# Optimization experiments

Hardware: AMD Instinct MI355X
Metric: run time of the kernel (lower is better)

The kernel has to match this reference:

```python
import jax, jax.numpy as jnp
import numpy as np

H = 8          # num_heads
EPS = 1e-5     # nn.LayerNorm default eps


def _attn(x, kv, wq, bq, wk, bk, wv, bv, wo, bo):
    # x: [B, Nq, D] queries; kv: [B, Nk, D] keys/values. softmax over keys (dim=-1).
    B, Nq, D = x.shape
    Nk = kv.shape[1]
    d = D // H
    q = (x @ wq + bq).reshape(B, Nq, H, d).transpose(0, 2, 1, 3)   # [B,h,Nq,d]
    k = (kv @ wk + bk).reshape(B, Nk, H, d).transpose(0, 2, 1, 3)  # [B,h,Nk,d]
    v = (kv @ wv + bv).reshape(B, Nk, H, d).transpose(0, 2, 1, 3)  # [B,h,Nk,d]
    scores = jnp.einsum('bhqd,bhkd->bhqk', q, k) * (d ** -0.5)
    a = jax.nn.softmax(scores, axis=-1)                            # softmax_dim='keys'
    ctx = jnp.einsum('bhqk,bhkd->bhqd', a, v)
    ctx = ctx.transpose(0, 2, 1, 3).reshape(B, Nq, D)
    return ctx @ wo + bo


def _ln(x, g, b):
    mu = jnp.mean(x, axis=-1, keepdims=True)
    var = jnp.var(x, axis=-1, keepdims=True)  # biased, matches torch LayerNorm
    return (x - mu) * jax.lax.rsqrt(var + EPS) * g + b


def setup_inputs() -> dict:
    key = jax.random.key(0)
    B, Nq, Nk, D = 2, 2048, 4096, 512
    Hid = 4 * D
    ks = jax.random.split(key, 32)
    s = 0.02
    r = lambda i, shp: jax.random.normal(ks[i], shp, dtype=jnp.float32) * s
    inp = {
        'x': jax.random.normal(ks[0], (B, Nq, D), dtype=jnp.float32),
        'cross': jax.random.normal(ks[1], (B, Nk, D), dtype=jnp.float32),
        # cross-attention projections (stored as [in, out])
        'ca_wq': r(2, (D, D)), 'ca_bq': jnp.zeros((D,), jnp.float32),
        'ca_wk': r(3, (D, D)), 'ca_bk': jnp.zeros((D,), jnp.float32),
        'ca_wv': r(4, (D, D)), 'ca_bv': jnp.zeros((D,), jnp.float32),
        'ca_wo': r(5, (D, D)), 'ca_bo': jnp.zeros((D,), jnp.float32),
        # self-attention projections
        'sa_wq': r(6, (D, D)), 'sa_bq': jnp.zeros((D,), jnp.float32),
        'sa_wk': r(7, (D, D)), 'sa_bk': jnp.zeros((D,), jnp.float32),
        'sa_wv': r(8, (D, D)), 'sa_bv': jnp.zeros((D,), jnp.float32),
        'sa_wo': r(9, (D, D)), 'sa_bo': jnp.zeros((D,), jnp.float32),
        # layer norms
        'ln1_g': jnp.ones((D,), jnp.float32), 'ln1_b': jnp.zeros((D,), jnp.float32),
        'ln2_g': jnp.ones((D,), jnp.float32), 'ln2_b': jnp.zeros((D,), jnp.float32),
        # MLP
        'mlp_w1': r(10, (D, Hid)), 'mlp_b1': jnp.zeros((Hid,), jnp.float32),
        'mlp_w2': r(11, (Hid, D)), 'mlp_b2': jnp.zeros((D,), jnp.float32),
    }
    return inp


def reference(x, cross,
              ca_wq, ca_bq, ca_wk, ca_bk, ca_wv, ca_bv, ca_wo, ca_bo,
              sa_wq, sa_bq, sa_wk, sa_bk, sa_wv, sa_bv, sa_wo, sa_bo,
              ln1_g, ln1_b, ln2_g, ln2_b,
              mlp_w1, mlp_b1, mlp_w2, mlp_b2):
    # a) cross-attention
    xc = _attn(x, cross, ca_wq, ca_bq, ca_wk, ca_bk, ca_wv, ca_bv, ca_wo, ca_bo)
    # b,c) LN then self-attention (Q=K=V=ln1(xc))
    xn = _ln(xc, ln1_g, ln1_b)
    xs = _attn(xn, xn, sa_wq, sa_bq, sa_wk, sa_bk, sa_wv, sa_bv, sa_wo, sa_bo)
    # d) residual
    y = xc + xs
    # e,f) LN + GELU MLP (torch GELU default = exact erf)
    h1 = jax.nn.gelu(_ln(y, ln2_g, ln2_b) @ mlp_w1 + mlp_b1, approximate=False)
    z = h1 @ mlp_w2 + mlp_b2
    # g) residual
    return y + z
```

## Files before the change

kernel.cpp:

```cpp
#include <hip/hip_runtime.h>
#include <math.h>

typedef _Float16 f16;
typedef __attribute__((ext_vector_type(8))) _Float16 f16x8;
typedef __attribute__((ext_vector_type(4))) _Float16 f16x4;
typedef __attribute__((ext_vector_type(4))) float f32x4;
typedef __attribute__((ext_vector_type(2))) __fp16 h16x2;

#define QSCALE 0.1803368801111204f

__device__ __forceinline__ void gl_lds16(const f16* g, f16* l) {
    __builtin_amdgcn_global_load_lds((const __attribute__((address_space(1))) void*)g,
                                     (__attribute__((address_space(3))) void*)l, 16, 0, 0);
}

struct PrepArgs {
    const float* ws[10]; f16* wd[10];
    const float* x; f16* xh;
    const float* cross; f16* ch;
};
__global__ __launch_bounds__(256)
void prep_all(PrepArgs p) {
    __shared__ float t[32][33];
    int bid = blockIdx.x, tid = threadIdx.x;
    if (bid < 4096) {
        const float* W; f16* Wt; int K, N, nx, ky;
        if (bid < 2048) {
            int wi = bid >> 8, tl = bid & 255;
            W = p.ws[wi]; Wt = p.wd[wi]; K = 512; N = 512; nx = tl & 15; ky = tl >> 4;
        } else if (bid < 3072) {
            int tl = bid - 2048;
            W = p.ws[8]; Wt = p.wd[8]; K = 512; N = 2048; nx = tl & 63; ky = tl >> 6;
        } else {
            int tl = bid - 3072;
            W = p.ws[9]; Wt = p.wd[9]; K = 2048; N = 512; nx = tl & 15; ky = tl >> 4;
        }
        int tx = tid & 31, ty = tid >> 5;
        int n0 = nx * 32, k0 = ky * 32;
#pragma unroll
        for (int i = 0; i < 4; i++)
            t[ty + i * 8][tx] = W[(size_t)(k0 + ty + i * 8) * N + n0 + tx];
        __syncthreads();
#pragma unroll
        for (int i = 0; i < 4; i++)
            Wt[(size_t)(n0 + ty + i * 8) * K + k0 + tx] = (f16)t[tx][ty + i * 8];
    } else {
        const float* X; f16* Y; size_t cb;
        if (bid < 6144) { X = p.x; Y = p.xh; cb = bid - 4096; }
        else            { X = p.cross; Y = p.ch; cb = bid - 6144; }
        size_t i = (cb * 256 + tid) * 4;
        f32x4 v = *(const f32x4*)(X + i);
        f16x4 o;
        o[0] = (f16)v[0]; o[1] = (f16)v[1]; o[2] = (f16)v[2]; o[3] = (f16)v[3];
        *(f16x4*)(Y + i) = o;
    }
}

__global__ __launch_bounds__(256)
void transpose_v(const f16* __restrict__ Vh, f16* __restrict__ Vt, int Nk) {
    __shared__ f16 t[64][72];
    int bh = blockIdx.y, k0 = blockIdx.x * 64;
    int tid = threadIdx.x;
    int kr = tid >> 2, dc = (tid & 3) * 16;
    const f16* src = Vh + ((size_t)bh * Nk + k0 + kr) * 64 + dc;
    f16x8 a = *(const f16x8*)src;
    f16x8 b = *(const f16x8*)(src + 8);
    *(f16x8*)&t[kr][dc] = a;
    *(f16x8*)&t[kr][dc + 8] = b;
    __syncthreads();
    int dr = tid >> 2, kc = (tid & 3) * 16;
    f16x8 o0, o1;
#pragma unroll
    for (int j = 0; j < 8; j++) { o0[j] = t[kc + j][dr]; o1[j] = t[kc + 8 + j][dr]; }
    f16* dst = Vt + ((size_t)bh * 64 + dr) * Nk + k0 + kc;
    *(f16x8*)dst = o0;
    *(f16x8*)(dst + 8) = o1;
}

__global__ __launch_bounds__(128)
void layernorm_f16(const float* __restrict__ X, const float* __restrict__ g,
                   const float* __restrict__ bta, f16* __restrict__ Y)
{
    __shared__ float red[4];
    int row = blockIdx.x;
    int tid = threadIdx.x;
    const float* x = X + (size_t)row * 512;
    f32x4 v = *(const f32x4*)(x + tid * 4);
    float s  = v[0] + v[1] + v[2] + v[3];
    float ss = v[0] * v[0] + v[1] * v[1] + v[2] * v[2] + v[3] * v[3];
#pragma unroll
    for (int m = 1; m < 64; m <<= 1) {
        s  += __shfl_xor(s, m, 64);
        ss += __shfl_xor(ss, m, 64);
    }
    int wave = tid >> 6, lane = tid & 63;
    if (lane == 0) { red[wave * 2] = s; red[wave * 2 + 1] = ss; }
    __syncthreads();
    s = red[0] + red[2]; ss = red[1] + red[3];
    float mu  = s * (1.0f / 512);
    float var = ss * (1.0f / 512) - mu * mu;
    float inv = rsqrtf(var + 1e-5f);
    f32x4 gv = *(const f32x4*)(g + tid * 4);
    f32x4 bv = *(const f32x4*)(bta + tid * 4);
    f16x4 o;
#pragma unroll
    for (int i = 0; i < 4; i++) o[i] = (f16)((v[i] - mu) * inv * gv[i] + bv[i]);
    *(f16x4*)(Y + (size_t)row * 512 + tid * 4) = o;
}

__global__ __launch_bounds__(256)
void gemm_f16(const f16* __restrict__ A, const f16* __restrict__ Wt,
              const float* __restrict__ b0, const float* __restrict__ b1,
              const float* __restrict__ b2, const float* __restrict__ res,
              float* __restrict__ Cf32, f16* __restrict__ C16,
              f16* __restrict__ hm0, f16* __restrict__ hm1, f16* __restrict__ hm2,
              int N, int K, int NBshift, int fused, int act, float s0)
{
    __shared__ __align__(16) f16 As[2][128 * 64];
    __shared__ __align__(16) f16 Bs[2][128 * 64];
    int tid = threadIdx.x, lane = tid & 63, wave = tid >> 6;
    int quad = lane >> 4, ln16 = lane & 15;
    int wm = wave >> 1, wn = wave & 1;
    int bm0 = blockIdx.y * 128, bn0 = blockIdx.x * 128;

    f32x4 acc[4][4];
#pragma unroll
    for (int i = 0; i < 4; i++)
#pragma unroll
        for (int j = 0; j < 4; j++) acc[i][j] = (f32x4){0.f, 0.f, 0.f, 0.f};

    const f16* ag[4]; const f16* bg[4]; int Loff[4];
#pragma unroll
    for (int j = 0; j < 4; j++) {
        int L = tid + j * 256;
        int row = L >> 3, cc = (L & 7) ^ (row & 7);
        ag[j] = A  + (size_t)(bm0 + row) * K + cc * 8;
        bg[j] = Wt + (size_t)(bn0 + row) * K + cc * 8;
        Loff[j] = L * 8;
    }
    int sw0 = (quad ^ (ln16 & 7)) * 8, sw1 = ((4 + quad) ^ (ln16 & 7)) * 8;

#pragma unroll
    for (int j = 0; j < 4; j++) { gl_lds16(ag[j], &As[0][Loff[j]]); gl_lds16(bg[j], &Bs[0][Loff[j]]); }
#pragma unroll
    for (int j = 0; j < 4; j++) { ag[j] += 64; bg[j] += 64; }

    int cur = 0;
    for (int kt = 0; kt < K; kt += 64) {
        __syncthreads();
        if (kt + 64 < K) {
            int nxt = cur ^ 1;
#pragma unroll
            for (int j = 0; j < 4; j++) { gl_lds16(ag[j], &As[nxt][Loff[j]]); gl_lds16(bg[j], &Bs[nxt][Loff[j]]); }
#pragma unroll
            for (int j = 0; j < 4; j++) { ag[j] += 64; bg[j] += 64; }
        }
        const f16* Ac = As[cur]; const f16* Bc = Bs[cur];
#pragma unroll
        for (int h = 0; h < 2; h++) {
            int sw = h ? sw1 : sw0;
            f16x8 af[4], bf[4];
#pragma unroll
            for (int mt = 0; mt < 4; mt++)
                af[mt] = *(const f16x8*)&Ac[(wm * 64 + mt * 16 + ln16) * 64 + sw];
#pragma unroll
            for (int nt = 0; nt < 4; nt++)
                bf[nt] = *(const f16x8*)&Bc[(wn * 64 + nt * 16 + ln16) * 64 + sw];
#pragma unroll
            for (int mt = 0; mt < 4; mt++)
#pragma unroll
                for (int nt = 0; nt < 4; nt++)
                    acc[mt][nt] = __builtin_amdgcn_mfma_f32_16x16x32_f16(af[mt], bf[nt], acc[mt][nt], 0, 0, 0);
        }
        cur ^= 1;
    }

    int NB = 1 << NBshift;
#pragma unroll
    for (int mt = 0; mt < 4; mt++) {
#pragma unroll
        for (int nt = 0; nt < 4; nt++) {
            int row = bm0 + wm * 64 + mt * 16 + quad * 4;
            int col = bn0 + wn * 64 + nt * 16 + ln16;
            float bv;
            if (fused) {
                int seg = col >> 9;
                const float* bp = seg == 0 ? b0 : (seg == 1 ? b1 : b2);
                bv = bp[col & 511];
            } else bv = b0[col];
#pragma unroll
            for (int i = 0; i < 4; i++) {
                int r = row + i;
                float v = acc[mt][nt][i] + bv;
                size_t idx = (size_t)r * N + col;
                if (res) v += res[idx];
                if (act) v = 0.5f * v * (1.0f + erff(v * 0.70710678118654752f));
                if (Cf32) Cf32[idx] = v;
                if (C16) C16[idx] = (f16)v;
                if (hm0) {
                    int seg = col >> 9;
                    f16* hp = seg == 0 ? hm0 : (seg == 1 ? hm1 : hm2);
                    float vv = seg == 0 ? v * s0 : v;
                    int hh = (col >> 6) & 7, d = col & 63;
                    int bt = r >> NBshift, rr = r & (NB - 1);
                    hp[(((size_t)bt * 8 + hh) * NB + rr) * 64 + d] = (f16)vv;
                }
            }
        }
    }
}

__global__ __launch_bounds__(256)
void gemm64(const f16* __restrict__ A, const f16* __restrict__ Wt,
            const float* __restrict__ bias, const float* __restrict__ res,
            float* __restrict__ Cf32, f16* __restrict__ hm0,
            int N, int K, int NBshift, float s0)
{
    __shared__ __align__(16) f16 As[2][64 * 64];
    __shared__ __align__(16) f16 Bs[2][64 * 64];
    int tid = threadIdx.x, lane = tid & 63, wave = tid >> 6;
    int quad = lane >> 4, ln16 = lane & 15;
    int wm = wave >> 1, wn = wave & 1;
    int bm0 = blockIdx.y * 64, bn0 = blockIdx.x * 64;

    f32x4 acc[2][2];
#pragma unroll
    for (int i = 0; i < 2; i++)
#pragma unroll
        for (int j = 0; j < 2; j++) acc[i][j] = (f32x4){0.f, 0.f, 0.f, 0.f};

    const f16* ag[2]; const f16* bg[2]; int Loff[2];
#pragma unroll
    for (int j = 0; j < 2; j++) {
        int L = tid + j * 256;
        int row = L >> 3, cc = (L & 7) ^ (row & 7);
        ag[j] = A  + (size_t)(bm0 + row) * K + cc * 8;
        bg[j] = Wt + (size_t)(bn0 + row) * K + cc * 8;
        Loff[j] = L * 8;
    }
    int sw0 = (quad ^ (ln16 & 7)) * 8, sw1 = ((4 + quad) ^ (ln16 & 7)) * 8;

#pragma unroll
    for (int j = 0; j < 2; j++) { gl_lds16(ag[j], &As[0][Loff[j]]); gl_lds16(bg[j], &Bs[0][Loff[j]]); }
#pragma unroll
    for (int j = 0; j < 2; j++) { ag[j] += 64; bg[j] += 64; }

    int cur = 0;
    for (int kt = 0; kt < K; kt += 64) {
        __syncthreads();
        if (kt + 64 < K) {
            int nxt = cur ^ 1;
#pragma unroll
            for (int j = 0; j < 2; j++) { gl_lds16(ag[j], &As[nxt][Loff[j]]); gl_lds16(bg[j], &Bs[nxt][Loff[j]]); }
#pragma unroll
            for (int j = 0; j < 2; j++) { ag[j] += 64; bg[j] += 64; }
        }
        const f16* Ac = As[cur]; const f16* Bc = Bs[cur];
#pragma unroll
        for (int h = 0; h < 2; h++) {
            int sw = h ? sw1 : sw0;
            f16x8 af[2], bf[2];
#pragma unroll
            for (int mt = 0; mt < 2; mt++)
                af[mt] = *(const f16x8*)&Ac[(wm * 32 + mt * 16 + ln16) * 64 + sw];
#pragma unroll
            for (int nt = 0; nt < 2; nt++)
                bf[nt] = *(const f16x8*)&Bc[(wn * 32 + nt * 16 + ln16) * 64 + sw];
#pragma unroll
            for (int mt = 0; mt < 2; mt++)
#pragma unroll
                for (int nt = 0; nt < 2; nt++)
                    acc[mt][nt] = __builtin_amdgcn_mfma_f32_16x16x32_f16(af[mt], bf[nt], acc[mt][nt], 0, 0, 0);
        }
        cur ^= 1;
    }

    int NB = 1 << NBshift;
#pragma unroll
    for (int mt = 0; mt < 2; mt++) {
#pragma unroll
        for (int nt = 0; nt < 2; nt++) {
            int row = bm0 + wm * 32 + mt * 16 + quad * 4;
            int col = bn0 + wn * 32 + nt * 16 + ln16;
            float bv = bias[col];
#pragma unroll
            for (int i = 0; i < 4; i++) {
                int r = row + i;
                float v = acc[mt][nt][i] + bv;
                size_t idx = (size_t)r * N + col;
                if (res) v += res[idx];
                if (Cf32) Cf32[idx] = v;
                if (hm0) {
                    int hh = (col >> 6) & 7, d = col & 63;
                    int bt = r >> NBshift, rr = r & (NB - 1);
                    hm0[(((size_t)bt * 8 + hh) * NB + rr) * 64 + d] = (f16)(v * s0);
                }
            }
        }
    }
}

__global__ __launch_bounds__(512, 4)
void attention_split(const f16* __restrict__ Qh, const f16* __restrict__ Kh,
                     const f16* __restrict__ Vt, f16* __restrict__ Op,
                     float* __restrict__ Lsum, int Nk)
{
    __shared__ __align__(16) f16 Kt[2][64 * 64];
    __shared__ __align__(16) f16 Vs[2][64 * 64];
    int z = blockIdx.z, b = z >> 2, sp = z & 3;
    int h = blockIdx.y, bh = b * 8 + h;
    int Nkh = Nk >> 2;
    int tid = threadIdx.x, lane = tid & 63, wave = tid >> 6;
    int quad = lane >> 4, ln16 = lane & 15, l7 = ln16 & 7;
    int qrow0 = blockIdx.x * 256 + wave * 32;

    f16x8 qf[2][2];
#pragma unroll
    for (int qh = 0; qh < 2; qh++)
#pragma unroll
        for (int dh = 0; dh < 2; dh++)
            qf[qh][dh] = *(const f16x8*)(Qh + ((size_t)bh * 2048 + qrow0 + qh * 16 + ln16) * 64
                                         + dh * 32 + quad * 8);
    f16x4 ones4;
#pragma unroll
    for (int j = 0; j < 4; j++) ones4[j] = (f16)1.0f;

    f32x4 oacc[2][4], aol[2];
#pragma unroll
    for (int qh = 0; qh < 2; qh++) {
        aol[qh] = (f32x4){0.f, 0.f, 0.f, 0.f};
#pragma unroll
        for (int dt = 0; dt < 4; dt++) oacc[qh][dt] = (f32x4){0.f, 0.f, 0.f, 0.f};
    }

    const f16* kb = Kh + ((size_t)bh * Nk + sp * Nkh) * 64;
    const f16* vb = Vt + (size_t)bh * 64 * Nk + sp * Nkh;

    const f16* kg; const f16* vg; int Lo;
    {
        int L = tid;
        int row = L >> 3, cc = (L & 7) ^ (row & 7);
        kg = kb + (size_t)row * 64 + cc * 8;
        vg = vb + (size_t)row * Nk + cc * 8;
        Lo = L * 8;
    }

    int koff[4][2], voff16[4][4];
#pragma unroll
    for (int nt = 0; nt < 4; nt++)
#pragma unroll
        for (int dh = 0; dh < 2; dh++)
            koff[nt][dh] = (nt * 16 + ln16) * 64 + ((dh * 4 + quad) ^ l7) * 8;
#pragma unroll
    for (int dt = 0; dt < 4; dt++)
#pragma unroll
        for (int nt = 0; nt < 4; nt++)
            voff16[dt][nt] = (dt * 16 + ln16) * 64 + (((nt * 2 + (quad >> 1)) ^ l7) * 8) + (quad & 1) * 4;

    gl_lds16(kg, &Kt[0][Lo]);
    gl_lds16(vg, &Vs[0][Lo]);
    kg += 64 * 64; vg += 64;

    int cur = 0;
    for (int kt = 0; kt < Nkh; kt += 64) {
        __syncthreads();
        if (kt + 64 < Nkh) {
            int nxt = cur ^ 1;
            gl_lds16(kg, &Kt[nxt][Lo]);
            gl_lds16(vg, &Vs[nxt][Lo]);
            kg += 64 * 64; vg += 64;
        }
        const f16* Ktc = Kt[cur]; const f16* Vsc = Vs[cur];

        f16x4 pk[2][4];
        {
            f16x8 kf[4][2];
#pragma unroll
            for (int nt = 0; nt < 4; nt++)
#pragma unroll
                for (int dh = 0; dh < 2; dh++)
                    kf[nt][dh] = *(const f16x8*)&Ktc[koff[nt][dh]];
#pragma unroll
            for (int qh = 0; qh < 2; qh++)
#pragma unroll
                for (int nt = 0; nt < 4; nt++) {
                    f32x4 zz = (f32x4){0.f, 0.f, 0.f, 0.f};
                    zz = __builtin_amdgcn_mfma_f32_16x16x32_f16(kf[nt][0], qf[qh][0], zz, 0, 0, 0);
                    zz = __builtin_amdgcn_mfma_f32_16x16x32_f16(kf[nt][1], qf[qh][1], zz, 0, 0, 0);
                    h16x2 pa = __builtin_amdgcn_cvt_pkrtz(exp2f(zz[0]), exp2f(zz[1]));
                    h16x2 pb = __builtin_amdgcn_cvt_pkrtz(exp2f(zz[2]), exp2f(zz[3]));
                    union { h16x2 h[2]; f16x4 v; } u;
                    u.h[0] = pa; u.h[1] = pb;
                    pk[qh][nt] = u.v;
                }
        }
        {
            f16x4 vf[4][4];
#pragma unroll
            for (int dt = 0; dt < 4; dt++)
#pragma unroll
                for (int nt = 0; nt < 4; nt++)
                    vf[dt][nt] = *(const f16x4*)&Vsc[voff16[dt][nt]];
#pragma unroll
            for (int qh = 0; qh < 2; qh++) {
#pragma unroll
                for (int nt = 0; nt < 4; nt++)
                    aol[qh] = __builtin_amdgcn_mfma_f32_16x16x16f16(ones4, pk[qh][nt], aol[qh], 0, 0, 0);
#pragma unroll
                for (int dt = 0; dt < 4; dt++)
#pragma unroll
                    for (int nt = 0; nt < 4; nt++)
                        oacc[qh][dt] = __builtin_amdgcn_mfma_f32_16x16x16f16(vf[dt][nt], pk[qh][nt], oacc[qh][dt], 0, 0, 0);
            }
        }
        cur ^= 1;
    }

#pragma unroll
    for (int qh = 0; qh < 2; qh++) {
        size_t rowb = ((size_t)(sp * 16 + bh) * 2048 + qrow0 + qh * 16 + ln16) * 64;
#pragma unroll
        for (int dt = 0; dt < 4; dt++) {
            f16x4 o4;
#pragma unroll
            for (int i = 0; i < 4; i++) o4[i] = (f16)oacc[qh][dt][i];
            *(f16x4*)&Op[rowb + dt * 16 + quad * 4] = o4;
        }
        if (quad == 0)
            Lsum[(size_t)(sp * 16 + bh) * 2048 + qrow0 + qh * 16 + ln16] = aol[qh][0];
    }
}

__global__ __launch_bounds__(256)
void attn_combine(const f16* __restrict__ Op, const float* __restrict__ Lsum,
                  f16* __restrict__ O)
{
    int t = blockIdx.x * 256 + threadIdx.x;
    int d = t & 63;
    int q = (t >> 6) & 2047;
    int bh = t >> 17;
    int b = bh >> 3, h = bh & 7;
    float l = 0.f, val = 0.f;
#pragma unroll
    for (int s = 0; s < 4; s++) {
        l   += Lsum[(size_t)(s * 16 + bh) * 2048 + q];
        val += (float)Op[((size_t)(s * 16 + bh) * 2048 + q) * 64 + d];
    }
    O[((size_t)b * 2048 + q) * 512 + h * 64 + d] = (f16)(val / l);
}

extern "C" void kernel_launch(void* const* d_in, const int* in_sizes, int n_in,
                              void* d_out, int out_size, void* d_ws, size_t ws_size,
                              hipStream_t stream)
{
    (void)in_sizes; (void)n_in; (void)out_size; (void)ws_size;
    const float* x      = (const float*)d_in[0];
    const float* cross  = (const float*)d_in[1];
    const float* ca_wq  = (const float*)d_in[2];
    const float* ca_bq  = (const float*)d_in[3];
    const float* ca_wk  = (const float*)d_in[4];
    const float* ca_bk  = (const float*)d_in[5];
    const float* ca_wv  = (const float*)d_in[6];
    const float* ca_bv  = (const float*)d_in[7];
    const float* ca_wo  = (const float*)d_in[8];
    const float* ca_bo  = (const float*)d_in[9];
    const float* sa_wq  = (const float*)d_in[10];
    const float* sa_bq  = (const float*)d_in[11];
    const float* sa_wk  = (const float*)d_in[12];
    const float* sa_bk  = (const float*)d_in[13];
    const float* sa_wv  = (const float*)d_in[14];
    const float* sa_bv  = (const float*)d_in[15];
    const float* sa_wo  = (const float*)d_in[16];
    const float* sa_bo  = (const float*)d_in[17];
    const float* ln1_g  = (const float*)d_in[18];
    const float* ln1_b  = (const float*)d_in[19];
    const float* ln2_g  = (const float*)d_in[20];
    const float* ln2_b  = (const float*)d_in[21];
    const float* mlp_w1 = (const float*)d_in[22];
    const float* mlp_b1 = (const float*)d_in[23];
    const float* mlp_w2 = (const float*)d_in[24];
    const float* mlp_b2 = (const float*)d_in[25];
    float* out = (float*)d_out;

    float* XC = (float*)d_ws;
    float* Yb = XC + 2097152;
    f16* fb   = (f16*)(Yb + 2097152);
    f16* xh     = fb;
    f16* crossh = xh + 2097152;
    f16* xnh    = crossh + 4194304;
    f16* xn2h   = xnh + 2097152;
    f16* Qh     = xn2h + 2097152;
    f16* Kh     = Qh + 2097152;
    f16* Vh     = Kh + 4194304;
    f16* Vtb    = Vh + 4194304;
    f16* ctxh   = Vtb + 4194304;
    f16* h1h    = ctxh + 2097152;
    f16* t_caq  = h1h + 8388608;
    f16* t_cak  = t_caq + 262144;
    f16* t_cav  = t_cak + 262144;
    f16* t_cao  = t_cav + 262144;
    f16* t_saq  = t_cao + 262144;
    f16* t_sak  = t_saq + 262144;
    f16* t_sav  = t_sak + 262144;
    f16* t_sao  = t_sav + 262144;
    f16* t_w1   = t_sao + 262144;
    f16* t_w2   = t_w1 + 1048576;
    float* Lsum = (float*)(t_w2 + 1048576);

    PrepArgs pa;
    pa.ws[0] = ca_wq; pa.wd[0] = t_caq;
    pa.ws[1] = ca_wk; pa.wd[1] = t_cak;
    pa.ws[2] = ca_wv; pa.wd[2] = t_cav;
    pa.ws[3] = ca_wo; pa.wd[3] = t_cao;
    pa.ws[4] = sa_wq; pa.wd[4] = t_saq;
    pa.ws[5] = sa_wk; pa.wd[5] = t_sak;
    pa.ws[6] = sa_wv; pa.wd[6] = t_sav;
    pa.ws[7] = sa_wo; pa.wd[7] = t_sao;
    pa.ws[8] = mlp_w1; pa.wd[8] = t_w1;
    pa.ws[9] = mlp_w2; pa.wd[9] = t_w2;
    pa.x = x; pa.xh = xh; pa.cross = cross; pa.ch = crossh;
    prep_all<<<10240, 256, 0, stream>>>(pa);

    gemm64<<<dim3(8, 64), 256, 0, stream>>>(xh, t_caq, ca_bq, nullptr, nullptr, Qh,
                                            512, 512, 11, QSCALE);
    gemm_f16<<<dim3(8, 64), 256, 0, stream>>>(crossh, t_cak, ca_bk, ca_bv, nullptr, nullptr,
        nullptr, nullptr, Kh, Vh, nullptr, 1024, 512, 12, 1, 0, 1.0f);
    transpose_v<<<dim3(64, 16), 256, 0, stream>>>(Vh, Vtb, 4096);
    attention_split<<<dim3(8, 8, 8), 512, 0, stream>>>(Qh, Kh, Vtb, h1h, Lsum, 4096);
    attn_combine<<<8192, 256, 0, stream>>>(h1h, Lsum, ctxh);
    gemm64<<<dim3(8, 64), 256, 0, stream>>>(ctxh, t_cao, ca_bo, nullptr, XC, nullptr,
                                            512, 512, 11, 1.0f);
    layernorm_f16<<<4096, 128, 0, stream>>>(XC, ln1_g, ln1_b, xnh);
    gemm_f16<<<dim3(12, 32), 256, 0, stream>>>(xnh, t_saq, sa_bq, sa_bk, sa_bv, nullptr,
        nullptr, nullptr, Qh, Kh, Vh, 1536, 512, 11, 1, 0, QSCALE);
    transpose_v<<<dim3(32, 16), 256, 0, stream>>>(Vh, Vtb, 2048);
    attention_split<<<dim3(8, 8, 8), 512, 0, stream>>>(Qh, Kh, Vtb, h1h, Lsum, 2048);
    attn_combine<<<8192, 256, 0, stream>>>(h1h, Lsum, ctxh);
    gemm64<<<dim3(8, 64), 256, 0, stream>>>(ctxh, t_sao, sa_bo, XC, Yb, nullptr,
                                            512, 512, 11, 1.0f);
    layernorm_f16<<<4096, 128, 0, stream>>>(Yb, ln2_g, ln2_b, xn2h);
    gemm_f16<<<dim3(16, 32), 256, 0, stream>>>(xn2h, t_w1, mlp_b1, nullptr, nullptr, nullptr,
        nullptr, h1h, nullptr, nullptr, nullptr, 2048, 512, 11, 0, 1, 1.0f);
    gemm64<<<dim3(8, 64), 256, 0, stream>>>(h1h, t_w2, mlp_b2, Yb, out, nullptr,
                                            512, 2048, 11, 1.0f);
}
```

Measured before the change: 361.1 us.

## Shrink attention blocks, swizzle grid for XCD locality, sum softmax denominators in VALU

```diff
diff --git a/kernel.cpp b/kernel.cpp
--- a/kernel.cpp
+++ b/kernel.cpp
@@ -300,19 +300,24 @@
     }
 }
 
-__global__ __launch_bounds__(512, 4)
+__global__ __launch_bounds__(256, 5)
 void attention_split(const f16* __restrict__ Qh, const f16* __restrict__ Kh,
                      const f16* __restrict__ Vt, f16* __restrict__ Op,
                      float* __restrict__ Lsum, int Nk)
 {
     __shared__ __align__(16) f16 Kt[2][64 * 64];
     __shared__ __align__(16) f16 Vs[2][64 * 64];
-    int z = blockIdx.z, b = z >> 2, sp = z & 3;
-    int h = blockIdx.y, bh = b * 8 + h;
+    int fid = blockIdx.x;
+    int xcd = fid & 7, slot = fid >> 3;
+    int c = xcd * 8 + (slot >> 4);
+    int qt = slot & 15;
+    int h = c & 7, z = c >> 3;
+    int b = z >> 2, sp = z & 3;
+    int bh = b * 8 + h;
     int Nkh = Nk >> 2;
     int tid = threadIdx.x, lane = tid & 63, wave = tid >> 6;
     int quad = lane >> 4, ln16 = lane & 15, l7 = ln16 & 7;
-    int qrow0 = blockIdx.x * 256 + wave * 32;
+    int qrow0 = qt * 128 + wave * 32;
 
     f16x8 qf[2][2];
 #pragma unroll
@@ -321,28 +326,25 @@
         for (int dh = 0; dh < 2; dh++)
             qf[qh][dh] = *(const f16x8*)(Qh + ((size_t)bh * 2048 + qrow0 + qh * 16 + ln16) * 64
                                          + dh * 32 + quad * 8);
-    f16x4 ones4;
-#pragma unroll
-    for (int j = 0; j < 4; j++) ones4[j] = (f16)1.0f;
-
-    f32x4 oacc[2][4], aol[2];
-#pragma unroll
-    for (int qh = 0; qh < 2; qh++) {
-        aol[qh] = (f32x4){0.f, 0.f, 0.f, 0.f};
+
+    f32x4 oacc[2][4];
+    float lacc[2] = {0.f, 0.f};
+#pragma unroll
+    for (int qh = 0; qh < 2; qh++)
 #pragma unroll
         for (int dt = 0; dt < 4; dt++) oacc[qh][dt] = (f32x4){0.f, 0.f, 0.f, 0.f};
-    }
 
     const f16* kb = Kh + ((size_t)bh * Nk + sp * Nkh) * 64;
     const f16* vb = Vt + (size_t)bh * 64 * Nk + sp * Nkh;
 
-    const f16* kg; const f16* vg; int Lo;
-    {
-        int L = tid;
+    const f16* kg[2]; const f16* vg[2]; int Lo[2];
+#pragma unroll
+    for (int j = 0; j < 2; j++) {
+        int L = tid + j * 256;
         int row = L >> 3, cc = (L & 7) ^ (row & 7);
-        kg = kb + (size_t)row * 64 + cc * 8;
-        vg = vb + (size_t)row * Nk + cc * 8;
-        Lo = L * 8;
+        kg[j] = kb + (size_t)row * 64 + cc * 8;
+        vg[j] = vb + (size_t)row * Nk + cc * 8;
+        Lo[j] = L * 8;
     }
 
     int koff[4][2], voff16[4][4];
@@ -357,18 +359,24 @@
         for (int nt = 0; nt < 4; nt++)
             voff16[dt][nt] = (dt * 16 + ln16) * 64 + (((nt * 2 + (quad >> 1)) ^ l7) * 8) + (quad & 1) * 4;
 
-    gl_lds16(kg, &Kt[0][Lo]);
-    gl_lds16(vg, &Vs[0][Lo]);
-    kg += 64 * 64; vg += 64;
+#pragma unroll
+    for (int j = 0; j < 2; j++) {
+        gl_lds16(kg[j], &Kt[0][Lo[j]]);
+        gl_lds16(vg[j], &Vs[0][Lo[j]]);
+        kg[j] += 64 * 64; vg[j] += 64;
+    }
 
     int cur = 0;
     for (int kt = 0; kt < Nkh; kt += 64) {
         __syncthreads();
         if (kt + 64 < Nkh) {
             int nxt = cur ^ 1;
-            gl_lds16(kg, &Kt[nxt][Lo]);
-            gl_lds16(vg, &Vs[nxt][Lo]);
-            kg += 64 * 64; vg += 64;
+#pragma unroll
+            for (int j = 0; j < 2; j++) {
+                gl_lds16(kg[j], &Kt[nxt][Lo[j]]);
+                gl_lds16(vg[j], &Vs[nxt][Lo[j]]);
+                kg[j] += 64 * 64; vg[j] += 64;
+            }
         }
         const f16* Ktc = Kt[cur]; const f16* Vsc = Vs[cur];
 
@@ -387,10 +395,13 @@
                     f32x4 zz = (f32x4){0.f, 0.f, 0.f, 0.f};
                     zz = __builtin_amdgcn_mfma_f32_16x16x32_f16(kf[nt][0], qf[qh][0], zz, 0, 0, 0);
                     zz = __builtin_amdgcn_mfma_f32_16x16x32_f16(kf[nt][1], qf[qh][1], zz, 0, 0, 0);
-                    h16x2 pa = __builtin_amdgcn_cvt_pkrtz(exp2f(zz[0]), exp2f(zz[1]));
-                    h16x2 pb = __builtin_amdgcn_cvt_pkrtz(exp2f(zz[2]), exp2f(zz[3]));
-                    union { h16x2 h[2]; f16x4 v; } u;
-                    u.h[0] = pa; u.h[1] = pb;
+                    float e0 = exp2f(zz[0]), e1 = exp2f(zz[1]);
+                    float e2 = exp2f(zz[2]), e3 = exp2f(zz[3]);
+                    lacc[qh] += (e0 + e1) + (e2 + e3);
+                    h16x2 pa = __builtin_amdgcn_cvt_pkrtz(e0, e1);
+                    h16x2 pb = __builtin_amdgcn_cvt_pkrtz(e2, e3);
+                    union { h16x2 hh[2]; f16x4 v; } u;
+                    u.hh[0] = pa; u.hh[1] = pb;
                     pk[qh][nt] = u.v;
                 }
         }
@@ -402,22 +413,21 @@
                 for (int nt = 0; nt < 4; nt++)
                     vf[dt][nt] = *(const f16x4*)&Vsc[voff16[dt][nt]];
 #pragma unroll
-            for (int qh = 0; qh < 2; qh++) {
-#pragma unroll
-                for (int nt = 0; nt < 4; nt++)
-                    aol[qh] = __builtin_amdgcn_mfma_f32_16x16x16f16(ones4, pk[qh][nt], aol[qh], 0, 0, 0);
+            for (int qh = 0; qh < 2; qh++)
 #pragma unroll
                 for (int dt = 0; dt < 4; dt++)
 #pragma unroll
                     for (int nt = 0; nt < 4; nt++)
                         oacc[qh][dt] = __builtin_amdgcn_mfma_f32_16x16x16f16(vf[dt][nt], pk[qh][nt], oacc[qh][dt], 0, 0, 0);
-            }
         }
         cur ^= 1;
     }
 
 #pragma unroll
     for (int qh = 0; qh < 2; qh++) {
+        float l = lacc[qh];
+        l += __shfl_xor(l, 16, 64);
+        l += __shfl_xor(l, 32, 64);
         size_t rowb = ((size_t)(sp * 16 + bh) * 2048 + qrow0 + qh * 16 + ln16) * 64;
 #pragma unroll
         for (int dt = 0; dt < 4; dt++) {
@@ -427,7 +437,7 @@
             *(f16x4*)&Op[rowb + dt * 16 + quad * 4] = o4;
         }
         if (quad == 0)
-            Lsum[(size_t)(sp * 16 + bh) * 2048 + qrow0 + qh * 16 + ln16] = aol[qh][0];
+            Lsum[(size_t)(sp * 16 + bh) * 2048 + qrow0 + qh * 16 + ln16] = l;
     }
 }
 
@@ -526,7 +536,7 @@
     gemm_f16<<<dim3(8, 64), 256, 0, stream>>>(crossh, t_cak, ca_bk, ca_bv, nullptr, nullptr,
         nullptr, nullptr, Kh, Vh, nullptr, 1024, 512, 12, 1, 0, 1.0f);
     transpose_v<<<dim3(64, 16), 256, 0, stream>>>(Vh, Vtb, 4096);
-    attention_split<<<dim3(8, 8, 8), 512, 0, stream>>>(Qh, Kh, Vtb, h1h, Lsum, 4096);
+    attention_split<<<1024, 256, 0, stream>>>(Qh, Kh, Vtb, h1h, Lsum, 4096);
     attn_combine<<<8192, 256, 0, stream>>>(h1h, Lsum, ctxh);
     gemm64<<<dim3(8, 64), 256, 0, stream>>>(ctxh, t_cao, ca_bo, nullptr, XC, nullptr,
                                             512, 512, 11, 1.0f);
@@ -534,7 +544,7 @@
     gemm_f16<<<dim3(12, 32), 256, 0, stream>>>(xnh, t_saq, sa_bq, sa_bk, sa_bv, nullptr,
         nullptr, nullptr, Qh, Kh, Vh, 1536, 512, 11, 1, 0, QSCALE);
     transpose_v<<<dim3(32, 16), 256, 0, stream>>>(Vh, Vtb, 2048);
-    attention_split<<<dim3(8, 8, 8), 512, 0, stream>>>(Qh, Kh, Vtb, h1h, Lsum, 2048);
+    attention_split<<<1024, 256, 0, stream>>>(Qh, Kh, Vtb, h1h, Lsum, 2048);
     attn_combine<<<8192, 256, 0, stream>>>(h1h, Lsum, ctxh);
     gemm64<<<dim3(8, 64), 256, 0, stream>>>(ctxh, t_sao, sa_bo, XC, Yb, nullptr,
                                             512, 512, 11, 1.0f);
```

Result: slower. 577.1 us (+59.8%).
